# Kernel tuning notes

Hardware: AMD Instinct MI355X
Metric: run time of the kernel (lower is better)

Reference implementation:

```python
import jax, jax.numpy as jnp
import numpy as np

K = 0.1  # curvature (called k in the module)
EPS = 1e-15

def setup_inputs() -> dict:
    key = jax.random.key(0)
    k1, k2, k3 = jax.random.split(key, 3)
    B, C, D = 2048, 1000, 64
    x = jax.random.normal(k1, (B, D), dtype=jnp.float32) * 0.05  # inside ball
    a_vals = jax.random.normal(k2, (C, D), dtype=jnp.float32) * 0.05
    p_vals = jax.random.normal(k3, (C, D), dtype=jnp.float32) * 0.05
    return {"x": x, "a_vals": a_vals, "p_vals": p_vals}

def reference(x, a_vals, p_vals):
    k = jnp.asarray(K, dtype=x.dtype)
    sqrt_k = jnp.sqrt(k)
    # poincare_exp0: exponential map at the origin
    p_norm = jnp.maximum(jnp.linalg.norm(p_vals, axis=1, keepdims=True), EPS)  # [C,1]
    p_poin = jnp.tanh(sqrt_k * p_norm) * p_vals / (sqrt_k * p_norm)            # [C,D]
    # conformal scaling of a (as written in the module: 1 + k*||p||^2)
    p2 = jnp.sum(p_poin * p_poin, axis=1)                                      # [C]
    a_poin = a_vals * (1.0 + k * p2)[:, None]                                  # [C,D]
    # hyperbolic softmax logits
    lam = 2.0 / (1.0 - k * p2)                                                 # [C]
    a_norm = jnp.maximum(jnp.linalg.norm(a_poin, axis=1), EPS)                 # [C]
    scale = lam * a_norm / sqrt_k                                              # [C]
    # mobius addition of (-p) (+) x, batched -> [C,B,D]
    mp = -p_poin                                                               # [C,D]
    xy = jnp.einsum('cd,bd->cb', mp, x)                                        # [C,B]
    x2 = jnp.sum(mp * mp, axis=-1)[:, None]                                    # [C,1]
    y2 = jnp.sum(x * x, axis=-1)[None, :]                                      # [1,B]
    num = ((1.0 + 2.0 * k * xy + k * y2)[..., None] * mp[:, None, :]
           + (1.0 - k * x2)[..., None] * x[None, :, :])                        # [C,B,D]
    den = 1.0 + 2.0 * k * xy + (k * k) * x2 * y2                               # [C,B]
    mob = num / den[..., None]                                                 # [C,B,D]
    numer = 2.0 * sqrt_k * jnp.einsum('cbd,cd->cb', mob, a_poin)               # [C,B]
    denom = a_norm[:, None] * (1.0 - k * jnp.sum(mob * mob, axis=-1))          # [C,B]
    logits = scale[:, None] * jnp.arcsinh(numer / denom)                       # [C,B]
    return logits.T                                                            # [B,C]
```

## Files before the change

kernel.cpp:

```cpp
#include <hip/hip_runtime.h>
#include <hip/hip_bf16.h>
#include <math.h>

#define KCURV  0.1f
#define KK     0.010000001f
#define SQRT_K 0.31622776601683794f
#define TWO_SQRT_K 0.6324555320336759f
#define INV_SQRT_K 3.1622776601683795f
#define TD 64

typedef __bf16  bf16x8  __attribute__((ext_vector_type(8)));
typedef float   f32x4   __attribute__((ext_vector_type(4)));

__device__ __forceinline__ unsigned short f2bf(float f) {
    __hip_bfloat16 h = __float2bfloat16(f);
    return *(unsigned short*)&h;
}

__global__ __launch_bounds__(256) void fused_mlr_kernel(
    const float* __restrict__ x,
    const float* __restrict__ a_vals,
    const float* __restrict__ p_vals,
    float* __restrict__ out, int B, int C)
{
    const int tid  = threadIdx.x;
    const int w    = tid >> 6;
    const int lane = tid & 63;
    const int m16  = lane & 15;
    const int quad = lane >> 4;
    const int cb   = blockIdx.x * 64;
    const int rb   = blockIdx.y * 64;
    int arow = rb + 16 * w + m16; if (arow >= B) arow = B - 1;

    float xv[2][8];
    #pragma unroll
    for (int step = 0; step < 2; ++step) {
        const int ko = quad * 8 + step * 32;
        const float* xr = x + (size_t)arow * TD + ko;
        *(float4*)&xv[step][0] = *(const float4*)xr;
        *(float4*)&xv[step][4] = *(const float4*)(xr + 4);
    }

    bf16x8 bp[4][2], ba[4][2];
    float x2s[4], pas[4], ans[4], scs[4];
    #pragma unroll
    for (int t = 0; t < 4; ++t) {
        int c = cb + 16 * t + m16; if (c >= C) c = C - 1;
        const float* pr = p_vals + (size_t)c * TD + quad * 8;
        const float* ar = a_vals + (size_t)c * TD + quad * 8;
        float pv[16], av[16];
        *(float4*)&pv[0]  = *(const float4*)pr;
        *(float4*)&pv[4]  = *(const float4*)(pr + 4);
        *(float4*)&pv[8]  = *(const float4*)(pr + 32);
        *(float4*)&pv[12] = *(const float4*)(pr + 36);
        *(float4*)&av[0]  = *(const float4*)ar;
        *(float4*)&av[4]  = *(const float4*)(ar + 4);
        *(float4*)&av[8]  = *(const float4*)(ar + 32);
        *(float4*)&av[12] = *(const float4*)(ar + 36);

        float s_pp = 0.f, s_aa = 0.f, s_pa = 0.f;
        #pragma unroll
        for (int u = 0; u < 16; ++u) {
            s_pp = fmaf(pv[u], pv[u], s_pp);
            s_aa = fmaf(av[u], av[u], s_aa);
            s_pa = fmaf(pv[u], av[u], s_pa);
        }
        s_pp += __shfl_xor(s_pp, 16, 64); s_pp += __shfl_xor(s_pp, 32, 64);
        s_aa += __shfl_xor(s_aa, 16, 64); s_aa += __shfl_xor(s_aa, 32, 64);
        s_pa += __shfl_xor(s_pa, 16, 64); s_pa += __shfl_xor(s_pa, 32, 64);

        float pn = sqrtf(s_pp); if (pn < 1e-15f) pn = 1e-15f;
        float arg = SQRT_K * pn;
        float e2 = __expf(2.0f * arg);
        float th = (e2 - 1.0f) * __builtin_amdgcn_rcpf(e2 + 1.0f);
        float factor = (arg > 1e-4f) ? th * __builtin_amdgcn_rcpf(arg)
                                     : 1.0f - 0.333333333f * arg * arg;
        float p2 = factor * factor * s_pp;
        float ca = 1.0f + KCURV * p2;
        float anorm = ca * sqrtf(s_aa); if (anorm < 1e-15f) anorm = 1e-15f;
        float lam = 2.0f * __builtin_amdgcn_rcpf(1.0f - KCURV * p2);
        x2s[t] = p2;
        pas[t] = -factor * ca * s_pa;
        ans[t] = anorm;
        scs[t] = lam * anorm * INV_SQRT_K;

        union { unsigned short u[8]; bf16x8 v; } c0, c1, d0, d1;
        #pragma unroll
        for (int u = 0; u < 8; ++u) {
            c0.u[u] = f2bf(-factor * pv[u]);
            c1.u[u] = f2bf(-factor * pv[8 + u]);
            d0.u[u] = f2bf(ca * av[u]);
            d1.u[u] = f2bf(ca * av[8 + u]);
        }
        bp[t][0] = c0.v; bp[t][1] = c1.v;
        ba[t][0] = d0.v; ba[t][1] = d1.v;
    }

    float s = 0.f;
    #pragma unroll
    for (int step = 0; step < 2; ++step)
        #pragma unroll
        for (int u = 0; u < 8; ++u) s = fmaf(xv[step][u], xv[step][u], s);
    s += __shfl_xor(s, 16, 64);
    s += __shfl_xor(s, 32, 64);
    float y2r[4];
    #pragma unroll
    for (int r = 0; r < 4; ++r) y2r[r] = __shfl(s, quad * 4 + r, 64);

    bf16x8 af[2];
    #pragma unroll
    for (int step = 0; step < 2; ++step) {
        union { unsigned short u[8]; bf16x8 v; } cv;
        #pragma unroll
        for (int u = 0; u < 8; ++u) cv.u[u] = f2bf(xv[step][u]);
        af[step] = cv.v;
    }

    f32x4 accP[4], accA[4];
    #pragma unroll
    for (int t = 0; t < 4; ++t) {
        accP[t] = (f32x4){0.f, 0.f, 0.f, 0.f};
        accA[t] = (f32x4){0.f, 0.f, 0.f, 0.f};
    }
    #pragma unroll
    for (int step = 0; step < 2; ++step) {
        #pragma unroll
        for (int t = 0; t < 4; ++t) {
            accP[t] = __builtin_amdgcn_mfma_f32_16x16x32_bf16(af[step], bp[t][step], accP[t], 0, 0, 0);
            accA[t] = __builtin_amdgcn_mfma_f32_16x16x32_bf16(af[step], ba[t][step], accA[t], 0, 0, 0);
        }
    }

    #pragma unroll
    for (int t = 0; t < 4; ++t) {
        const int cl = cb + 16 * t + m16;
        const float x2 = x2s[t], pa = pas[t], an = ans[t], sc = scs[t];
        const float beta = 1.0f - KCURV * x2;
        const float kkx2 = KK * x2;
        #pragma unroll
        for (int r = 0; r < 4; ++r) {
            const int gr = rb + 16 * w + quad * 4 + r;
            const float y2 = y2r[r];
            const float xy = accP[t][r];
            const float xa = accA[t][r];
            float t1    = fmaf(2.0f * KCURV, xy, 1.0f);
            float den   = fmaf(kkx2, y2, t1);
            float alpha = fmaf(KCURV, y2, t1);
            float g     = fmaf(alpha, pa, beta * xa);
            float M     = fmaf(alpha * alpha, x2,
                          fmaf(2.0f * alpha * beta, xy, beta * beta * y2));
            float dd    = fmaf(den, den, -KCURV * M);
            float z     = TWO_SQRT_K * g * den * __builtin_amdgcn_rcpf(an * dd);
            float lg    = sc * __logf(z + sqrtf(fmaf(z, z, 1.0f)));
            if (cl < C && gr < B) out[(size_t)gr * C + cl] = lg;
        }
    }
}

extern "C" void kernel_launch(void* const* d_in, const int* in_sizes, int n_in,
                              void* d_out, int out_size, void* d_ws, size_t ws_size,
                              hipStream_t stream) {
    const float* x      = (const float*)d_in[0];
    const float* a_vals = (const float*)d_in[1];
    const float* p_vals = (const float*)d_in[2];
    const int B = in_sizes[0] / TD;
    const int C = in_sizes[1] / TD;
    const int rowBlocks = (B + 63) / 64;
    const int clsBlocks = (C + 63) / 64;

    dim3 grid(clsBlocks, rowBlocks);
    fused_mlr_kernel<<<grid, dim3(256), 0, stream>>>(
        x, a_vals, p_vals, (float*)d_out, B, C);
}
```

Measured before the change: 75.06 us.

## Share per-class preprocessing across warps via LDS instead of recomputing per warp

```diff
diff --git a/kernel.cpp b/kernel.cpp
--- a/kernel.cpp
+++ b/kernel.cpp
@@ -8,6 +8,7 @@
 #define TWO_SQRT_K 0.6324555320336759f
 #define INV_SQRT_K 3.1622776601683795f
 #define TD 64
+#define LDP 72
 
 typedef __bf16  bf16x8  __attribute__((ext_vector_type(8)));
 typedef float   f32x4   __attribute__((ext_vector_type(4)));
@@ -23,6 +24,10 @@
     const float* __restrict__ p_vals,
     float* __restrict__ out, int B, int C)
 {
+    __shared__ unsigned short Pl[64 * LDP];
+    __shared__ unsigned short Al[64 * LDP];
+    __shared__ float scal[4][64];
+
     const int tid  = threadIdx.x;
     const int w    = tid >> 6;
     const int lane = tid & 63;
@@ -41,23 +46,18 @@
         *(float4*)&xv[step][4] = *(const float4*)(xr + 4);
     }
 
-    bf16x8 bp[4][2], ba[4][2];
-    float x2s[4], pas[4], ans[4], scs[4];
-    #pragma unroll
-    for (int t = 0; t < 4; ++t) {
-        int c = cb + 16 * t + m16; if (c >= C) c = C - 1;
-        const float* pr = p_vals + (size_t)c * TD + quad * 8;
-        const float* ar = a_vals + (size_t)c * TD + quad * 8;
+    {
+        const int ci = tid >> 2;
+        const int q  = tid & 3;
+        int c = cb + ci; if (c >= C) c = C - 1;
+        const float* pr = p_vals + (size_t)c * TD + q * 16;
+        const float* ar = a_vals + (size_t)c * TD + q * 16;
         float pv[16], av[16];
-        *(float4*)&pv[0]  = *(const float4*)pr;
-        *(float4*)&pv[4]  = *(const float4*)(pr + 4);
-        *(float4*)&pv[8]  = *(const float4*)(pr + 32);
-        *(float4*)&pv[12] = *(const float4*)(pr + 36);
-        *(float4*)&av[0]  = *(const float4*)ar;
-        *(float4*)&av[4]  = *(const float4*)(ar + 4);
-        *(float4*)&av[8]  = *(const float4*)(ar + 32);
-        *(float4*)&av[12] = *(const float4*)(ar + 36);
-
+        #pragma unroll
+        for (int m = 0; m < 4; ++m) {
+            *(float4*)&pv[m * 4] = *(const float4*)(pr + m * 4);
+            *(float4*)&av[m * 4] = *(const float4*)(ar + m * 4);
+        }
         float s_pp = 0.f, s_aa = 0.f, s_pa = 0.f;
         #pragma unroll
         for (int u = 0; u < 16; ++u) {
@@ -65,9 +65,9 @@
             s_aa = fmaf(av[u], av[u], s_aa);
             s_pa = fmaf(pv[u], av[u], s_pa);
         }
-        s_pp += __shfl_xor(s_pp, 16, 64); s_pp += __shfl_xor(s_pp, 32, 64);
-        s_aa += __shfl_xor(s_aa, 16, 64); s_aa += __shfl_xor(s_aa, 32, 64);
-        s_pa += __shfl_xor(s_pa, 16, 64); s_pa += __shfl_xor(s_pa, 32, 64);
+        s_pp += __shfl_xor(s_pp, 1, 64); s_pp += __shfl_xor(s_pp, 2, 64);
+        s_aa += __shfl_xor(s_aa, 1, 64); s_aa += __shfl_xor(s_aa, 2, 64);
+        s_pa += __shfl_xor(s_pa, 1, 64); s_pa += __shfl_xor(s_pa, 2, 64);
 
         float pn = sqrtf(s_pp); if (pn < 1e-15f) pn = 1e-15f;
         float arg = SQRT_K * pn;
@@ -79,21 +79,36 @@
         float ca = 1.0f + KCURV * p2;
         float anorm = ca * sqrtf(s_aa); if (anorm < 1e-15f) anorm = 1e-15f;
         float lam = 2.0f * __builtin_amdgcn_rcpf(1.0f - KCURV * p2);
-        x2s[t] = p2;
-        pas[t] = -factor * ca * s_pa;
-        ans[t] = anorm;
-        scs[t] = lam * anorm * INV_SQRT_K;
+        if (q == 0) {
+            scal[0][ci] = p2;
+            scal[1][ci] = -factor * ca * s_pa;
+            scal[2][ci] = anorm;
+            scal[3][ci] = lam * anorm * INV_SQRT_K;
+        }
+        unsigned short ubp[16], uba[16];
+        #pragma unroll
+        for (int u = 0; u < 16; ++u) {
+            ubp[u] = f2bf(-factor * pv[u]);
+            uba[u] = f2bf(ca * av[u]);
+        }
+        unsigned short* dp = &Pl[ci * LDP + q * 16];
+        unsigned short* da = &Al[ci * LDP + q * 16];
+        *(ulonglong2*)dp       = *(const ulonglong2*)&ubp[0];
+        *(ulonglong2*)(dp + 8) = *(const ulonglong2*)&ubp[8];
+        *(ulonglong2*)da       = *(const ulonglong2*)&uba[0];
+        *(ulonglong2*)(da + 8) = *(const ulonglong2*)&uba[8];
+    }
+    __syncthreads();
 
-        union { unsigned short u[8]; bf16x8 v; } c0, c1, d0, d1;
+    bf16x8 bp[4][2], ba[4][2];
+    #pragma unroll
+    for (int step = 0; step < 2; ++step) {
         #pragma unroll
-        for (int u = 0; u < 8; ++u) {
-            c0.u[u] = f2bf(-factor * pv[u]);
-            c1.u[u] = f2bf(-factor * pv[8 + u]);
-            d0.u[u] = f2bf(ca * av[u]);
-            d1.u[u] = f2bf(ca * av[8 + u]);
+        for (int t = 0; t < 4; ++t) {
+            const int off = (16 * t + m16) * LDP + quad * 8 + step * 32;
+            bp[t][step] = *(const bf16x8*)&Pl[off];
+            ba[t][step] = *(const bf16x8*)&Al[off];
         }
-        bp[t][0] = c0.v; bp[t][1] = c1.v;
-        ba[t][0] = d0.v; ba[t][1] = d1.v;
     }
 
     float s = 0.f;
@@ -134,7 +149,9 @@
     #pragma unroll
     for (int t = 0; t < 4; ++t) {
         const int cl = cb + 16 * t + m16;
-        const float x2 = x2s[t], pa = pas[t], an = ans[t], sc = scs[t];
+        const int si = 16 * t + m16;
+        const float x2 = scal[0][si], pa = scal[1][si];
+        const float an = scal[2][si], sc = scal[3][si];
         const float beta = 1.0f - KCURV * x2;
         const float kkx2 = KK * x2;
         #pragma unroll
```

Measured after the change: 65.18 us. 13.2% less time.
